# Kernel optimization log

Measured on AMD Instinct MI355X. Metric: run time of the kernel, lower is better.

Reference implementation:

```python
import jax, jax.numpy as jnp
import numpy as np

N_NODES = 100000


def setup_inputs() -> dict:
    key = jax.random.key(0)
    k1, k2, k3 = jax.random.split(key, 3)
    emb = jax.random.normal(k1, (N_NODES, 64), dtype=jnp.float32)
    src = jax.random.randint(k2, (1250000,), 0, N_NODES, dtype=jnp.int64)
    dst = jax.random.randint(k3, (1250000,), 0, N_NODES, dtype=jnp.int64)
    return {"emb": emb, "src": src, "dst": dst}


def reference(emb, src, dst):
    # DGL GraphConv(norm='both', weight=False, bias=False):
    #   out = D_in^{-1/2} * A * (D_out^{-1/2} * emb), degrees clamped to >= 1.
    n = emb.shape[0]
    e = src.shape[0]
    ones = jnp.ones((e,), dtype=emb.dtype)
    out_deg = jax.ops.segment_sum(ones, src, num_segments=n)  # out-degree of src nodes
    in_deg = jax.ops.segment_sum(ones, dst, num_segments=n)   # in-degree of dst nodes
    src_norm = jnp.clip(out_deg, 1.0, None) ** -0.5           # [N]
    dst_norm = jnp.clip(in_deg, 1.0, None) ** -0.5            # [N]
    h = emb * src_norm[:, None]                               # [N, D] pre-normalize
    msg = h[src]                                              # [E, D] gather
    agg = jax.ops.segment_sum(msg, dst, num_segments=n)       # [N, D] scatter-add
    return agg * dst_norm[:, None]
```

## Files before the change

kernel.cpp:

```cpp
#include <hip/hip_runtime.h>
#include <hip/hip_fp16.h>

#define NNODES 100000
#define DIM 64
#define TILE 256
#define NTILES ((NNODES + TILE - 1) / TILE)
#define NTPAD 392
#define CAP 4608
#define EPT 16
#define BIN_THREADS 512
#define BIN_CHUNK (BIN_THREADS * EPT)

__global__ __launch_bounds__(BIN_THREADS) void bin_kernel(
        const int* __restrict__ src, const int* __restrict__ dst,
        int* __restrict__ gcurD, int* __restrict__ gcurS,
        unsigned int* __restrict__ binnedD, int* __restrict__ binnedS, int E) {
    __shared__ int histD[NTPAD], histS[NTPAD], baseD[NTPAD], baseS[NTPAD];
    __shared__ unsigned short rankD[BIN_CHUNK], rankS[BIN_CHUNK];
    int tid = threadIdx.x;
    for (int t = tid; t < NTPAD; t += BIN_THREADS) { histD[t] = 0; histS[t] = 0; }
    __syncthreads();
    int base = blockIdx.x * BIN_CHUNK;
    #pragma unroll
    for (int i = 0; i < EPT; i++) {
        int idx = base + i * BIN_THREADS + tid;
        if (idx < E) {
            int d = dst[idx];
            int s = src[idx];
            rankD[i * BIN_THREADS + tid] = (unsigned short)atomicAdd(&histD[d >> 8], 1);
            rankS[i * BIN_THREADS + tid] = (unsigned short)atomicAdd(&histS[s >> 8], 1);
        }
    }
    __syncthreads();
    for (int t = tid; t < NTPAD; t += BIN_THREADS) {
        int h = histD[t];
        baseD[t] = h ? atomicAdd(&gcurD[t], h) : 0;
        h = histS[t];
        baseS[t] = h ? atomicAdd(&gcurS[t], h) : 0;
    }
    __syncthreads();
    #pragma unroll
    for (int i = 0; i < EPT; i++) {
        int idx = base + i * BIN_THREADS + tid;
        if (idx < E) {
            int d = dst[idx];
            int s = src[idx];
            int tD = d >> 8, tS = s >> 8;
            int pD = baseD[tD] + (int)rankD[i * BIN_THREADS + tid];
            int pS = baseS[tS] + (int)rankS[i * BIN_THREADS + tid];
            if (pD < CAP) binnedD[(size_t)tD * CAP + pD] = ((unsigned)(d & 255) << 17) | (unsigned)s;
            if (pS < CAP) binnedS[(size_t)tS * CAP + pS] = s;
        }
    }
}

__global__ __launch_bounds__(256) void sortnorm_kernel(
        const int* __restrict__ gcurS, const int* __restrict__ binnedS,
        const int* __restrict__ gcurD, const unsigned int* __restrict__ binnedD,
        const float* __restrict__ emb, __half* __restrict__ embh,
        int* __restrict__ sortedD, int* __restrict__ offs, int* __restrict__ deg) {
    __shared__ int cnt[TILE];
    __shared__ int cur[TILE];
    __shared__ float norm_s[TILE];
    __shared__ int wsum[4];
    __shared__ int tot_s;
    int t = blockIdx.x, tid = threadIdx.x;
    int node = t * TILE + tid;
    cnt[tid] = 0;
    __syncthreads();
    {
        int lenS = min(gcurS[t], CAP);
        const int* segS = binnedS + (size_t)t * CAP;
        for (int j = tid; j < lenS; j += 256)
            atomicAdd(&cnt[segS[j] & 255], 1);
    }
    __syncthreads();
    norm_s[tid] = rsqrtf(fmaxf((float)cnt[tid], 1.0f));
    __syncthreads();
    {
        int nrows = min(TILE, NNODES - t * TILE);
        size_t ebase = (size_t)t * TILE * DIM;
        int chunks = nrows * (DIM / 8);
        for (int i = tid; i < chunks; i += 256) {
            int off8 = i * 8;
            float w = norm_s[off8 >> 6];
            float4 a = *(const float4*)(emb + ebase + off8);
            float4 b = *(const float4*)(emb + ebase + off8 + 4);
            __half2* o = (__half2*)(embh + ebase + off8);
            o[0] = __floats2half2_rn(a.x * w, a.y * w);
            o[1] = __floats2half2_rn(a.z * w, a.w * w);
            o[2] = __floats2half2_rn(b.x * w, b.y * w);
            o[3] = __floats2half2_rn(b.z * w, b.w * w);
        }
        if (node == NNODES) {
            __half2 z = __floats2half2_rn(0.0f, 0.0f);
            __half2* o = (__half2*)(embh + (size_t)NNODES * DIM);
            #pragma unroll
            for (int k = 0; k < DIM / 2; k++) o[k] = z;
        }
    }
    __syncthreads();
    cnt[tid] = 0;
    __syncthreads();
    int len = min(gcurD[t], CAP);
    const unsigned int* seg = binnedD + (size_t)t * CAP;
    for (int j = tid; j < len; j += 256)
        atomicAdd(&cnt[seg[j] >> 17], 1);
    __syncthreads();
    int v = cnt[tid];
    int vpad = (v + 7) & ~7;
    int lane = tid & 63, w = tid >> 6;
    int x = vpad;
    #pragma unroll
    for (int off = 1; off < 64; off <<= 1) {
        int y = __shfl_up(x, off, 64);
        if (lane >= off) x += y;
    }
    if (lane == 63) wsum[w] = x;
    __syncthreads();
    int add = 0;
    #pragma unroll
    for (int k = 0; k < 4; k++) add += (k < w) ? wsum[k] : 0;
    int ex = x - vpad + add;
    cur[tid] = ex;
    if (tid == 255) tot_s = ex + vpad;
    __syncthreads();
    for (int j = tid; j < len; j += 256) {
        unsigned int p = seg[j];
        int dl = p >> 17;
        int pos = atomicAdd(&cur[dl], 1);
        if (pos < CAP) sortedD[(size_t)t * CAP + pos] = (int)(p & 0x1FFFF);
    }
    __syncthreads();
    int pe = ex + vpad;
    for (int p = cur[tid]; p < pe && p < CAP; p++) sortedD[(size_t)t * CAP + p] = NNODES;
    for (int k = tot_s + tid; k < CAP; k += 256) sortedD[(size_t)t * CAP + k] = NNODES;
    if (node < NNODES) {
        offs[node] = t * CAP + ex;
        deg[node] = v;
    }
}

__global__ __launch_bounds__(256) void agg4_kernel(
        const __half* __restrict__ embh, const int* __restrict__ offs,
        const int* __restrict__ deg, const int* __restrict__ sortedD,
        float* __restrict__ out, int n) {
    int wid = threadIdx.x >> 6;
    int lane = threadIdx.x & 63;
    int node = blockIdx.x * 4 + wid;
    if (node >= n) return;
    int m = deg[node];
    int mp = (m + 7) & ~7;
    const int* run = sortedD + offs[node];
    int slot = lane >> 3;
    int oct = lane & 7;
    float a0 = 0.f, a1 = 0.f, a2 = 0.f, a3 = 0.f, a4 = 0.f, a5 = 0.f, a6 = 0.f, a7 = 0.f;
    for (int j = 0; j < mp; j += 16) {
        int i0 = run[j + slot];
        int j2 = j + 8;
        int i1 = (j2 < mp) ? run[j2 + slot] : NNODES;
        float4 hv0 = *(const float4*)(embh + ((size_t)i0 << 6) + (oct << 3));
        float4 hv1 = *(const float4*)(embh + ((size_t)i1 << 6) + (oct << 3));
        const __half2* h0 = (const __half2*)&hv0;
        const __half2* h1 = (const __half2*)&hv1;
        float2 f;
        f = __half22float2(h0[0]); a0 += f.x; a1 += f.y;
        f = __half22float2(h0[1]); a2 += f.x; a3 += f.y;
        f = __half22float2(h0[2]); a4 += f.x; a5 += f.y;
        f = __half22float2(h0[3]); a6 += f.x; a7 += f.y;
        f = __half22float2(h1[0]); a0 += f.x; a1 += f.y;
        f = __half22float2(h1[1]); a2 += f.x; a3 += f.y;
        f = __half22float2(h1[2]); a4 += f.x; a5 += f.y;
        f = __half22float2(h1[3]); a6 += f.x; a7 += f.y;
    }
    #pragma unroll
    for (int off = 8; off < 64; off <<= 1) {
        a0 += __shfl_xor(a0, off);
        a1 += __shfl_xor(a1, off);
        a2 += __shfl_xor(a2, off);
        a3 += __shfl_xor(a3, off);
        a4 += __shfl_xor(a4, off);
        a5 += __shfl_xor(a5, off);
        a6 += __shfl_xor(a6, off);
        a7 += __shfl_xor(a7, off);
    }
    float dn = rsqrtf(fmaxf((float)m, 1.0f));
    if (lane < 16) {
        int half = lane >> 3;
        float4 o = half ? make_float4(a4 * dn, a5 * dn, a6 * dn, a7 * dn)
                        : make_float4(a0 * dn, a1 * dn, a2 * dn, a3 * dn);
        *(float4*)(out + ((size_t)node << 6) + (oct << 3) + (half << 2)) = o;
    }
}

extern "C" void kernel_launch(void* const* d_in, const int* in_sizes, int n_in,
                              void* d_out, int out_size, void* d_ws, size_t ws_size,
                              hipStream_t stream) {
    const float* emb = (const float*)d_in[0];
    const int* src = (const int*)d_in[1];
    const int* dst = (const int*)d_in[2];
    int E = in_sizes[1];
    float* out = (float*)d_out;

    int* gcurD = (int*)d_ws;
    int* gcurS = gcurD + NTPAD;
    unsigned int* binnedD = (unsigned int*)(gcurS + NTPAD);
    int* binnedS = (int*)(binnedD + (size_t)NTILES * CAP);
    int* sortedD = binnedS;
    int* offs = binnedS + (size_t)NTILES * CAP;
    int* deg = offs + NNODES;
    __half* embh = (__half*)(deg + NNODES);

    hipMemsetAsync(gcurD, 0, 2 * NTPAD * sizeof(int), stream);

    int bin_blocks = (E + BIN_CHUNK - 1) / BIN_CHUNK;
    bin_kernel<<<bin_blocks, BIN_THREADS, 0, stream>>>(src, dst, gcurD, gcurS, binnedD, binnedS, E);

    sortnorm_kernel<<<NTILES, 256, 0, stream>>>(gcurS, binnedS, gcurD, binnedD,
                                                emb, embh, sortedD, offs, deg);

    agg4_kernel<<<(NNODES + 3) / 4, 256, 0, stream>>>(embh, offs, deg, sortedD, out, NNODES);
}
```

Baseline: 99.97 us.

## Split half-precision table into column slabs and aggregate per slab

The pre-normalized fp16 embedding table is stored as four 16-column slabs, each a contiguous array of 32-byte rows, instead of one interleaved 128-byte-per-row layout. The aggregation kernel now gives each block one slab, and each wave handles 8 nodes with 4 edge slots and 2 half-row lanes. Each pass over a slab touches a 3.2 MB table, which should fit in cache better and improve gather locality. Accumulation now uses fp16 __hadd2 rather than fp32, which risks precision loss or overflow for high-degree nodes, and the index lists are read once per slab (four times in total).

```diff
diff --git a/kernel.cpp b/kernel.cpp
--- a/kernel.cpp
+++ b/kernel.cpp
@@ -10,6 +10,7 @@
 #define EPT 16
 #define BIN_THREADS 512
 #define BIN_CHUNK (BIN_THREADS * EPT)
+#define NPAIR 4
 
 __global__ __launch_bounds__(BIN_THREADS) void bin_kernel(
         const int* __restrict__ src, const int* __restrict__ dst,
@@ -57,7 +58,7 @@
 __global__ __launch_bounds__(256) void sortnorm_kernel(
         const int* __restrict__ gcurS, const int* __restrict__ binnedS,
         const int* __restrict__ gcurD, const unsigned int* __restrict__ binnedD,
-        const float* __restrict__ emb, __half* __restrict__ embh,
+        const float* __restrict__ emb, __half* __restrict__ embp,
         int* __restrict__ sortedD, int* __restrict__ offs, int* __restrict__ deg) {
     __shared__ int cnt[TILE];
     __shared__ int cur[TILE];
@@ -79,24 +80,36 @@
     __syncthreads();
     {
         int nrows = min(TILE, NNODES - t * TILE);
+        int chunks = nrows * NPAIR;
         size_t ebase = (size_t)t * TILE * DIM;
-        int chunks = nrows * (DIM / 8);
         for (int i = tid; i < chunks; i += 256) {
-            int off8 = i * 8;
-            float w = norm_s[off8 >> 6];
-            float4 a = *(const float4*)(emb + ebase + off8);
-            float4 b = *(const float4*)(emb + ebase + off8 + 4);
-            __half2* o = (__half2*)(embh + ebase + off8);
+            int row = i >> 2;
+            int pair = i & 3;
+            const float* ep = emb + ebase + (size_t)row * DIM + pair * 16;
+            float w = norm_s[row];
+            float4 a = *(const float4*)(ep);
+            float4 b = *(const float4*)(ep + 4);
+            float4 c = *(const float4*)(ep + 8);
+            float4 d4 = *(const float4*)(ep + 12);
+            int gnode = t * TILE + row;
+            __half2* o = (__half2*)(embp + ((size_t)pair * (NNODES + 1) + gnode) * 16);
             o[0] = __floats2half2_rn(a.x * w, a.y * w);
             o[1] = __floats2half2_rn(a.z * w, a.w * w);
             o[2] = __floats2half2_rn(b.x * w, b.y * w);
             o[3] = __floats2half2_rn(b.z * w, b.w * w);
+            o[4] = __floats2half2_rn(c.x * w, c.y * w);
+            o[5] = __floats2half2_rn(c.z * w, c.w * w);
+            o[6] = __floats2half2_rn(d4.x * w, d4.y * w);
+            o[7] = __floats2half2_rn(d4.z * w, d4.w * w);
         }
         if (node == NNODES) {
             __half2 z = __floats2half2_rn(0.0f, 0.0f);
-            __half2* o = (__half2*)(embh + (size_t)NNODES * DIM);
             #pragma unroll
-            for (int k = 0; k < DIM / 2; k++) o[k] = z;
+            for (int p = 0; p < NPAIR; p++) {
+                __half2* o = (__half2*)(embp + ((size_t)p * (NNODES + 1) + NNODES) * 16);
+                #pragma unroll
+                for (int k = 0; k < 8; k++) o[k] = z;
+            }
         }
     }
     __syncthreads();
@@ -141,40 +154,46 @@
     }
 }
 
-__global__ __launch_bounds__(256) void agg4_kernel(
-        const __half* __restrict__ embh, const int* __restrict__ offs,
+__global__ __launch_bounds__(256) void agg6_kernel(
+        const __half* __restrict__ embp, const int* __restrict__ offs,
         const int* __restrict__ deg, const int* __restrict__ sortedD,
-        float* __restrict__ out, int n) {
+        float* __restrict__ out) {
+    int bid = blockIdx.x;
+    int pair = bid & 3;
+    int g = bid >> 2;
     int wid = threadIdx.x >> 6;
     int lane = threadIdx.x & 63;
-    int node = blockIdx.x * 4 + wid;
-    if (node >= n) return;
+    int nodesub = lane >> 3;
+    int slot = (lane >> 1) & 3;
+    int hl = lane & 1;
+    int node = g * 32 + wid * 8 + nodesub;
+    if (node >= NNODES) return;
     int m = deg[node];
     int mp = (m + 7) & ~7;
     const int* run = sortedD + offs[node];
-    int slot = lane >> 3;
-    int oct = lane & 7;
-    float a0 = 0.f, a1 = 0.f, a2 = 0.f, a3 = 0.f, a4 = 0.f, a5 = 0.f, a6 = 0.f, a7 = 0.f;
-    for (int j = 0; j < mp; j += 16) {
+    const __half* tbl = embp + (size_t)pair * (NNODES + 1) * 16;
+    __half2 hz = __floats2half2_rn(0.0f, 0.0f);
+    __half2 h0 = hz, h1 = hz, h2 = hz, h3 = hz;
+    for (int j = 0; j < mp; j += 8) {
         int i0 = run[j + slot];
-        int j2 = j + 8;
-        int i1 = (j2 < mp) ? run[j2 + slot] : NNODES;
-        float4 hv0 = *(const float4*)(embh + ((size_t)i0 << 6) + (oct << 3));
-        float4 hv1 = *(const float4*)(embh + ((size_t)i1 << 6) + (oct << 3));
-        const __half2* h0 = (const __half2*)&hv0;
-        const __half2* h1 = (const __half2*)&hv1;
-        float2 f;
-        f = __half22float2(h0[0]); a0 += f.x; a1 += f.y;
-        f = __half22float2(h0[1]); a2 += f.x; a3 += f.y;
-        f = __half22float2(h0[2]); a4 += f.x; a5 += f.y;
-        f = __half22float2(h0[3]); a6 += f.x; a7 += f.y;
-        f = __half22float2(h1[0]); a0 += f.x; a1 += f.y;
-        f = __half22float2(h1[1]); a2 += f.x; a3 += f.y;
-        f = __half22float2(h1[2]); a4 += f.x; a5 += f.y;
-        f = __half22float2(h1[3]); a6 += f.x; a7 += f.y;
-    }
-    #pragma unroll
-    for (int off = 8; off < 64; off <<= 1) {
+        int i1 = run[j + 4 + slot];
+        float4 v0 = *(const float4*)(tbl + ((size_t)i0 << 4) + (hl << 3));
+        float4 v1 = *(const float4*)(tbl + ((size_t)i1 << 4) + (hl << 3));
+        const __half2* p0 = (const __half2*)&v0;
+        const __half2* p1 = (const __half2*)&v1;
+        h0 = __hadd2(h0, p0[0]); h1 = __hadd2(h1, p0[1]);
+        h2 = __hadd2(h2, p0[2]); h3 = __hadd2(h3, p0[3]);
+        h0 = __hadd2(h0, p1[0]); h1 = __hadd2(h1, p1[1]);
+        h2 = __hadd2(h2, p1[2]); h3 = __hadd2(h3, p1[3]);
+    }
+    float2 f0 = __half22float2(h0);
+    float2 f1 = __half22float2(h1);
+    float2 f2 = __half22float2(h2);
+    float2 f3 = __half22float2(h3);
+    float a0 = f0.x, a1 = f0.y, a2 = f1.x, a3 = f1.y;
+    float a4 = f2.x, a5 = f2.y, a6 = f3.x, a7 = f3.y;
+    #pragma unroll
+    for (int off = 2; off <= 4; off <<= 1) {
         a0 += __shfl_xor(a0, off);
         a1 += __shfl_xor(a1, off);
         a2 += __shfl_xor(a2, off);
@@ -185,11 +204,10 @@
         a7 += __shfl_xor(a7, off);
     }
     float dn = rsqrtf(fmaxf((float)m, 1.0f));
-    if (lane < 16) {
-        int half = lane >> 3;
-        float4 o = half ? make_float4(a4 * dn, a5 * dn, a6 * dn, a7 * dn)
-                        : make_float4(a0 * dn, a1 * dn, a2 * dn, a3 * dn);
-        *(float4*)(out + ((size_t)node << 6) + (oct << 3) + (half << 2)) = o;
+    if (slot == 0) {
+        float* op = out + ((size_t)node << 6) + (pair << 4) + (hl << 3);
+        *(float4*)(op) = make_float4(a0 * dn, a1 * dn, a2 * dn, a3 * dn);
+        *(float4*)(op + 4) = make_float4(a4 * dn, a5 * dn, a6 * dn, a7 * dn);
     }
 }
 
@@ -209,7 +227,7 @@
     int* sortedD = binnedS;
     int* offs = binnedS + (size_t)NTILES * CAP;
     int* deg = offs + NNODES;
-    __half* embh = (__half*)(deg + NNODES);
+    __half* embp = (__half*)(deg + NNODES);
 
     hipMemsetAsync(gcurD, 0, 2 * NTPAD * sizeof(int), stream);
 
@@ -217,7 +235,8 @@
     bin_kernel<<<bin_blocks, BIN_THREADS, 0, stream>>>(src, dst, gcurD, gcurS, binnedD, binnedS, E);
 
     sortnorm_kernel<<<NTILES, 256, 0, stream>>>(gcurS, binnedS, gcurD, binnedD,
-                                                emb, embh, sortedD, offs, deg);
-
-    agg4_kernel<<<(NNODES + 3) / 4, 256, 0, stream>>>(embh, offs, deg, sortedD, out, NNODES);
-}
+                                                emb, embp, sortedD, offs, deg);
+
+    int ngroups = (NNODES + 31) / 32;
+    agg6_kernel<<<ngroups * NPAIR, 256, 0, stream>>>(embp, offs, deg, sortedD, out);
+}
```

Result: faster. 94.53 us (-5.4%).
